# Performance work log

Measured on AMD Instinct MI355X. Metric: run time of the kernel, lower is better.

The kernel has to match this reference:

```python
import math
import jax, jax.numpy as jnp
import numpy as np

B, S, D_MODEL, H = 2, 2048, 1024, 16
HD = D_MODEL // H  # head_dim = 64


def setup_inputs() -> dict:
    key = jax.random.key(0)
    ks = jax.random.split(key, 5)
    scale = 1.0 / math.sqrt(D_MODEL)
    return {
        "x": jax.random.normal(ks[0], (B, S, D_MODEL), dtype=jnp.float32),
        "attention_mask": jnp.ones((B, S), dtype=jnp.int32),
        "causal": 1,
        "Wq": jax.random.normal(ks[1], (D_MODEL, D_MODEL), dtype=jnp.float32) * scale,
        "Wk": jax.random.normal(ks[2], (D_MODEL, D_MODEL), dtype=jnp.float32) * scale,
        "Wv": jax.random.normal(ks[3], (D_MODEL, D_MODEL), dtype=jnp.float32) * scale,
        "Wo": jax.random.normal(ks[4], (D_MODEL, D_MODEL), dtype=jnp.float32) * scale,
    }


def reference(x, attention_mask, causal, Wq, Wk, Wv, Wo):
    b, s, d = x.shape
    # QKV projections, split heads -> (b, h, s, hd)
    q = (x @ Wq).reshape(b, s, H, HD).transpose(0, 2, 1, 3)
    k = (x @ Wk).reshape(b, s, H, HD).transpose(0, 2, 1, 3)
    v = (x @ Wv).reshape(b, s, H, HD).transpose(0, 2, 1, 3)

    score = jnp.einsum("bhqd,bhkd->bhqk", q, k) / math.sqrt(HD)

    neg_inf = jnp.float32(-jnp.inf)
    if causal:
        causal_mask = jnp.tril(jnp.ones((s, s), dtype=bool))  # (s, s)
        score = jnp.where(causal_mask[None, None, :, :], score, neg_inf)
    key_mask = attention_mask.astype(bool)[:, None, None, :]  # (b,1,1,s)
    score = jnp.where(key_mask, score, neg_inf)

    attn = jax.nn.softmax(score, axis=-1)  # numerically stable (max-subtracted)
    out = jnp.einsum("bhqk,bhkd->bhqd", attn, v)  # (b,h,s,hd)
    out = out.transpose(0, 2, 1, 3).reshape(b, s, d)
    return out @ Wo
```

## Files before the change

### kernel.cpp

```cpp
#include <hip/hip_runtime.h>
#include <hip/hip_bf16.h>

#define B_  2
#define S_  2048
#define D_  1024
#define H_  16
#define HD_ 64
#define BS_ (B_*S_)

typedef __attribute__((ext_vector_type(8))) short bf16x8;
typedef __attribute__((ext_vector_type(4))) float f32x4;
typedef __attribute__((ext_vector_type(4))) float float4v;
typedef __attribute__((ext_vector_type(4))) unsigned short ushort4v;
typedef __attribute__((ext_vector_type(2))) unsigned int uint2v;

__device__ __forceinline__ unsigned short f2bf(float f) {
  union { float f; unsigned int u; } v; v.f = f;
  unsigned int u = v.u;
  return (unsigned short)((u + 0x7fffu + ((u >> 16) & 1u)) >> 16);
}
__device__ __forceinline__ float bf2f(unsigned short u) {
  union { unsigned int i; float f; } v; v.i = ((unsigned int)u) << 16; return v.f;
}
__device__ __forceinline__ unsigned int cvtpk(float lo, float hi) {
  unsigned int r;
  asm("v_cvt_pk_bf16_f32 %0, %1, %2" : "=v"(r) : "v"(lo), "v"(hi));
  return r;
}

__device__ __forceinline__ void gload16(const void* g, void* l) {
  __builtin_amdgcn_global_load_lds((const __attribute__((address_space(1))) void*)g,
                                   (__attribute__((address_space(3))) void*)l, 16, 0, 0);
}

__device__ __forceinline__ f32x4 mfma16(bf16x8 a, bf16x8 b, f32x4 c) {
  return __builtin_amdgcn_mfma_f32_16x16x32_bf16(a, b, c, 0, 0, 0);
}

__device__ __forceinline__ void store1(float* p, float v) { *p = v; }
__device__ __forceinline__ void store1(unsigned short* p, float v) { *p = f2bf(v); }

__global__ __launch_bounds__(256) void k_convert(const float* __restrict__ src,
                                                 unsigned short* __restrict__ dst, int n8) {
  int i = blockIdx.x * 256 + threadIdx.x;
  if (i >= n8) return;
  float4v a = ((const float4v*)src)[2*i];
  float4v b = ((const float4v*)src)[2*i + 1];
  union { bf16x8 v; unsigned short u[8]; } o;
#pragma unroll
  for (int j = 0; j < 4; ++j) { o.u[j] = f2bf(a[j]); o.u[4+j] = f2bf(b[j]); }
  ((bf16x8*)dst)[i] = o.v;
}

__global__ __launch_bounds__(256) void k_wt(const float* __restrict__ w0, const float* __restrict__ w1,
                                            const float* __restrict__ w2, const float* __restrict__ w3,
                                            unsigned short* __restrict__ o0, unsigned short* __restrict__ o1,
                                            unsigned short* __restrict__ o2, unsigned short* __restrict__ o3) {
  const float* w = blockIdx.z == 0 ? w0 : blockIdx.z == 1 ? w1 : blockIdx.z == 2 ? w2 : w3;
  unsigned short* o = blockIdx.z == 0 ? o0 : blockIdx.z == 1 ? o1 : blockIdx.z == 2 ? o2 : o3;
  __shared__ unsigned short til[64][68];
  const int n0 = blockIdx.x * 64, k0 = blockIdx.y * 64;
  const int t = threadIdx.x, r = t >> 4, c4 = t & 15;
#pragma unroll
  for (int i = 0; i < 4; ++i) {
    float4v v = *(const float4v*)(w + (size_t)(k0 + i*16 + r) * D_ + n0 + c4*4);
#pragma unroll
    for (int j = 0; j < 4; ++j) til[i*16 + r][c4*4 + j] = f2bf(v[j]);
  }
  __syncthreads();
#pragma unroll
  for (int i = 0; i < 4; ++i) {
    ushort4v u;
#pragma unroll
    for (int j = 0; j < 4; ++j) u[j] = til[c4*4 + j][i*16 + r];
    *(ushort4v*)(o + (size_t)(n0 + i*16 + r) * D_ + k0 + c4*4) = u;
  }
}

template <typename OutT>
__device__ __forceinline__ void gemm_body(const unsigned short* __restrict__ A,
                                          const unsigned short* __restrict__ Bt,
                                          OutT* __restrict__ C,
                                          int M, int N, int K, int mblk, int nblk) {
  __shared__ unsigned short As[128 * 64];
  __shared__ unsigned short Bs[128 * 64];
  const int tid = threadIdx.x;
  const int w = tid >> 6, lane = tid & 63;
  const int lg = lane >> 4, li = lane & 15;
  const int m0 = mblk * 128, n0 = nblk * 128;
  const int wr = (w >> 1) * 64, wc = (w & 1) * 64;
  f32x4 acc[4][4] = {};
  for (int kt = 0; kt < K; kt += 64) {
#pragma unroll
    for (int i = 0; i < 4; ++i) {
      int c = (i*4 + w) * 64 + lane;
      int r = c >> 3, kc = c & 7;
      int off = ((kc ^ (r & 7)) << 3);
      gload16(A  + (size_t)(m0 + r) * K + kt + off, (char*)As + (i*4 + w) * 1024);
      gload16(Bt + (size_t)(n0 + r) * K + kt + off, (char*)Bs + (i*4 + w) * 1024);
    }
    __syncthreads();
#pragma unroll
    for (int ks = 0; ks < 2; ++ks) {
      bf16x8 af[4], bfr[4];
#pragma unroll
      for (int m = 0; m < 4; ++m) {
        int rr = wr + m*16 + li;
        int ch = (ks*4 + lg) ^ (rr & 7);
        af[m] = *(const bf16x8*)((const char*)As + rr*128 + ch*16);
      }
#pragma unroll
      for (int n = 0; n < 4; ++n) {
        int rr = wc + n*16 + li;
        int ch = (ks*4 + lg) ^ (rr & 7);
        bfr[n] = *(const bf16x8*)((const char*)Bs + rr*128 + ch*16);
      }
#pragma unroll
      for (int m = 0; m < 4; ++m)
#pragma unroll
        for (int n = 0; n < 4; ++n)
          acc[m][n] = mfma16(af[m], bfr[n], acc[m][n]);
    }
    __syncthreads();
  }
#pragma unroll
  for (int m = 0; m < 4; ++m)
#pragma unroll
    for (int n = 0; n < 4; ++n)
#pragma unroll
      for (int j = 0; j < 4; ++j) {
        int row = m0 + wr + m*16 + lg*4 + j;
        int col = n0 + wc + n*16 + li;
        store1(&C[(size_t)row * N + col], acc[m][n][j]);
      }
}

__global__ __launch_bounds__(256, 2) void k_qkv(const unsigned short* __restrict__ xb,
    const unsigned short* __restrict__ wqt, const unsigned short* __restrict__ wkt,
    const unsigned short* __restrict__ wvt,
    unsigned short* __restrict__ Qb, unsigned short* __restrict__ Kb, unsigned short* __restrict__ Vb) {
  const unsigned short* Bt = blockIdx.z == 0 ? wqt : blockIdx.z == 1 ? wkt : wvt;
  unsigned short* C = blockIdx.z == 0 ? Qb : blockIdx.z == 1 ? Kb : Vb;
  gemm_body<unsigned short>(xb, Bt, C, BS_, D_, D_, blockIdx.x, blockIdx.y);
}

__global__ __launch_bounds__(256, 2) void k_out(const unsigned short* __restrict__ AO,
                                                const unsigned short* __restrict__ wot,
                                                float* __restrict__ out) {
  gemm_body<float>(AO, wot, out, BS_, D_, D_, blockIdx.x, blockIdx.y);
}

__global__ __launch_bounds__(256) void k_vt(const unsigned short* __restrict__ V,
                                            unsigned short* __restrict__ Vt) {
  __shared__ unsigned short til[64][68];
  const int s0 = blockIdx.x * 64, bh = blockIdx.y;
  const int b = bh >> 4, h = bh & 15;
  const int t = threadIdx.x, r = t >> 4, c4 = t & 15;
#pragma unroll
  for (int i = 0; i < 4; ++i) {
    ushort4v v = *(const ushort4v*)(V + (size_t)(b*S_ + s0 + i*16 + r) * D_ + h*HD_ + c4*4);
#pragma unroll
    for (int j = 0; j < 4; ++j) til[i*16 + r][c4*4 + j] = v[j];
  }
  __syncthreads();
#pragma unroll
  for (int i = 0; i < 4; ++i) {
    ushort4v u;
#pragma unroll
    for (int j = 0; j < 4; ++j) u[j] = til[c4*4 + j][i*16 + r];
    *(ushort4v*)(Vt + (size_t)(bh*HD_ + i*16 + r) * S_ + s0 + c4*4) = u;
  }
}

__global__ __launch_bounds__(256, 4) void k_attn(const unsigned short* __restrict__ Q,
                                                 const unsigned short* __restrict__ K,
                                                 const unsigned short* __restrict__ Vt,
                                                 unsigned short* __restrict__ AO) {
  __shared__ unsigned short Ks[2 * 64 * 64];
  __shared__ unsigned short Vs[2 * 64 * 64];
  __shared__ unsigned short Ps[4 * 16 * 64];
  const int bh = blockIdx.x;
  const int qb = 31 - blockIdx.y;
  const int b = bh >> 4, h = bh & 15;
  const int tid = threadIdx.x, w = tid >> 6, lane = tid & 63;
  const int lg = lane >> 4, li = lane & 15;
  unsigned short* Psw = Ps + w * 1024;
  const float SC2 = 0.18033688f;

  const unsigned short* qptr = Q + (size_t)(b*S_ + qb*64 + w*16 + li) * D_ + h*HD_;
  union { bf16x8 v; unsigned short u[8]; } q0u, q1u;
  q0u.v = *(const bf16x8*)(qptr + lg*8);
  q1u.v = *(const bf16x8*)(qptr + 32 + lg*8);
#pragma unroll
  for (int j = 0; j < 8; ++j) {
    q0u.u[j] = f2bf(bf2f(q0u.u[j]) * SC2);
    q1u.u[j] = f2bf(bf2f(q1u.u[j]) * SC2);
  }
  const bf16x8 qf0 = q0u.v, qf1 = q1u.v;

  int paddr[8];
#pragma unroll
  for (int kj = 0; kj < 4; ++kj)
#pragma unroll
    for (int hh = 0; hh < 2; ++hh)
      paddr[kj*2 + hh] = li*128 + (((2*kj + (lg >> 1)) ^ (li & 7)) << 4) + (lg & 1)*8 + 4*hh;
  int pboff[2];
#pragma unroll
  for (int ks = 0; ks < 2; ++ks)
    pboff[ks] = li*128 + (((ks*4 + lg) ^ (li & 7)) << 4);

  f32x4 oacc[4] = {};
  float mrow = -1e30f, lrow = 0.f;

  auto stage = [&](int bsel, int kt) {
    char* KsB = (char*)Ks + bsel * 8192;
    char* VsB = (char*)Vs + bsel * 8192;
#pragma unroll
    for (int i = 0; i < 2; ++i) {
      int c = (i*4 + w) * 64 + lane;
      int r = c >> 3, kc = c & 7;
      int off = ((kc ^ (r & 7)) << 3);
      gload16(K  + (size_t)(b*S_ + kt*64 + r) * D_ + h*HD_ + off, KsB + (i*4 + w) * 1024);
      gload16(Vt + (size_t)(bh*HD_ + r) * S_ + kt*64 + off,       VsB + (i*4 + w) * 1024);
    }
  };

  stage(0, 0);
  __syncthreads();

  for (int kt = 0; kt <= qb; ++kt) {
    const int cur = kt & 1;
    if (kt < qb) stage(cur ^ 1, kt + 1);
    const char* KsB = (const char*)Ks + cur * 8192;
    const char* VsB = (const char*)Vs + cur * 8192;

    f32x4 sc[4];
    __builtin_amdgcn_s_setprio(1);
#pragma unroll
    for (int kj = 0; kj < 4; ++kj) {
      f32x4 t = {};
      t = mfma16(*(const bf16x8*)(KsB + kj*2048 + pboff[0]), qf0, t);
      t = mfma16(*(const bf16x8*)(KsB + kj*2048 + pboff[1]), qf1, t);
      sc[kj] = t;
    }
    __builtin_amdgcn_s_setprio(0);

    if (kt == qb) {
      const int qloc = w*16 + li;
#pragma unroll
      for (int kj = 0; kj < 4; ++kj)
#pragma unroll
        for (int j = 0; j < 4; ++j)
          if (kj*16 + lg*4 + j > qloc) sc[kj][j] = -1e30f;
    }

    float mx = sc[0][0];
#pragma unroll
    for (int kj = 0; kj < 4; ++kj)
#pragma unroll
      for (int j = 0; j < 4; ++j) mx = fmaxf(mx, sc[kj][j]);
    mx = fmaxf(mx, __shfl_xor(mx, 16, 64));
    mx = fmaxf(mx, __shfl_xor(mx, 32, 64));
    const float mnew = fmaxf(mrow, mx);
    if (__any(mnew != mrow)) {
      const float alpha = exp2f(mrow - mnew);
#pragma unroll
      for (int n = 0; n < 4; ++n)
#pragma unroll
        for (int j = 0; j < 4; ++j) oacc[n][j] *= alpha;
      lrow *= alpha;
      mrow = mnew;
    }
    float rs = 0.f;
    f32x4 pv[4];
#pragma unroll
    for (int kj = 0; kj < 4; ++kj)
#pragma unroll
      for (int j = 0; j < 4; ++j) {
        float p = exp2f(sc[kj][j] - mrow);
        rs += p;
        pv[kj][j] = p;
      }
    rs += __shfl_xor(rs, 16, 64);
    rs += __shfl_xor(rs, 32, 64);
    lrow += rs;

#pragma unroll
    for (int kj = 0; kj < 4; ++kj) {
      *(unsigned int*)((char*)Psw + paddr[kj*2 + 0]) = cvtpk(pv[kj][0], pv[kj][1]);
      *(unsigned int*)((char*)Psw + paddr[kj*2 + 1]) = cvtpk(pv[kj][2], pv[kj][3]);
    }

    const bf16x8 pf0 = *(const bf16x8*)((const char*)Psw + pboff[0]);
    const bf16x8 pf1 = *(const bf16x8*)((const char*)Psw + pboff[1]);
    __builtin_amdgcn_s_setprio(1);
#pragma unroll
    for (int n = 0; n < 4; ++n) {
      oacc[n] = mfma16(*(const bf16x8*)(VsB + n*2048 + pboff[0]), pf0, oacc[n]);
      oacc[n] = mfma16(*(const bf16x8*)(VsB + n*2048 + pboff[1]), pf1, oacc[n]);
    }
    __builtin_amdgcn_s_setprio(0);
    __syncthreads();
  }

  const float inv = 1.0f / lrow;
  unsigned short* aorow = AO + (size_t)(b*S_ + qb*64 + w*16 + li) * D_ + h*HD_;
#pragma unroll
  for (int n = 0; n < 4; ++n) {
    uint2v o2;
    o2[0] = cvtpk(oacc[n][0] * inv, oacc[n][1] * inv);
    o2[1] = cvtpk(oacc[n][2] * inv, oacc[n][3] * inv);
    *(uint2v*)(aorow + n*16 + lg*4) = o2;
  }
}

extern "C" void kernel_launch(void* const* d_in, const int* in_sizes, int n_in,
                              void* d_out, int out_size, void* d_ws, size_t ws_size,
                              hipStream_t stream) {
  const float* x  = (const float*)d_in[0];
  const float* Wq = (const float*)d_in[3];
  const float* Wk = (const float*)d_in[4];
  const float* Wv = (const float*)d_in[5];
  const float* Wo = (const float*)d_in[6];
  float* out = (float*)d_out;

  unsigned short* ws  = (unsigned short*)d_ws;
  unsigned short* xb  = ws;
  unsigned short* wqt = xb  + (size_t)BS_ * D_;
  unsigned short* wkt = wqt + (size_t)D_ * D_;
  unsigned short* wvt = wkt + (size_t)D_ * D_;
  unsigned short* wot = wvt + (size_t)D_ * D_;
  unsigned short* Qb  = wot + (size_t)D_ * D_;
  unsigned short* Kb  = Qb  + (size_t)BS_ * D_;
  unsigned short* Vb  = Kb  + (size_t)BS_ * D_;
  unsigned short* Vtb = Vb  + (size_t)BS_ * D_;
  unsigned short* AO  = Vtb + (size_t)BS_ * D_;

  k_convert<<<2048, 256, 0, stream>>>(x, xb, BS_ * D_ / 8);
  k_wt<<<dim3(16, 16, 4), 256, 0, stream>>>(Wq, Wk, Wv, Wo, wqt, wkt, wvt, wot);
  k_qkv<<<dim3(32, 8, 3), 256, 0, stream>>>(xb, wqt, wkt, wvt, Qb, Kb, Vb);
  k_vt<<<dim3(32, 32), 256, 0, stream>>>(Vb, Vtb);
  k_attn<<<dim3(32, 32), 256, 0, stream>>>(Qb, Kb, Vtb, AO);
  k_out<<<dim3(32, 8), 256, 0, stream>>>(AO, wot, out);
}
```

Baseline: 115.7 us.

## Fuse prep kernels, write V transposed from GEMM, and tune attention softmax

Merges the x conversion and weight transpose kernels into one launch. The QKV GEMM now writes V directly in transposed per-head layout, which removes the separate V-transpose kernel and its extra memory round trip. The attention kernel reorders q-block scheduling to balance causal work, precomputes load offsets, uses a lazy max-rescale threshold, and defers row-sum cross-lane reduction to the end. The lazy rescale lets exponents grow by up to 2^8 before rescaling, which is a small numerical risk, and the transposed V stores are narrow strided writes.

Result: faster. 112.4 us (-2.8%).

```diff
diff --git a/kernel.cpp b/kernel.cpp
--- a/kernel.cpp
+++ b/kernel.cpp
@@ -37,29 +37,28 @@
   return __builtin_amdgcn_mfma_f32_16x16x32_bf16(a, b, c, 0, 0, 0);
 }
 
-__device__ __forceinline__ void store1(float* p, float v) { *p = v; }
-__device__ __forceinline__ void store1(unsigned short* p, float v) { *p = f2bf(v); }
-
-__global__ __launch_bounds__(256) void k_convert(const float* __restrict__ src,
-                                                 unsigned short* __restrict__ dst, int n8) {
-  int i = blockIdx.x * 256 + threadIdx.x;
-  if (i >= n8) return;
-  float4v a = ((const float4v*)src)[2*i];
-  float4v b = ((const float4v*)src)[2*i + 1];
-  union { bf16x8 v; unsigned short u[8]; } o;
-#pragma unroll
-  for (int j = 0; j < 4; ++j) { o.u[j] = f2bf(a[j]); o.u[4+j] = f2bf(b[j]); }
-  ((bf16x8*)dst)[i] = o.v;
-}
-
-__global__ __launch_bounds__(256) void k_wt(const float* __restrict__ w0, const float* __restrict__ w1,
-                                            const float* __restrict__ w2, const float* __restrict__ w3,
-                                            unsigned short* __restrict__ o0, unsigned short* __restrict__ o1,
-                                            unsigned short* __restrict__ o2, unsigned short* __restrict__ o3) {
-  const float* w = blockIdx.z == 0 ? w0 : blockIdx.z == 1 ? w1 : blockIdx.z == 2 ? w2 : w3;
-  unsigned short* o = blockIdx.z == 0 ? o0 : blockIdx.z == 1 ? o1 : blockIdx.z == 2 ? o2 : o3;
+__global__ __launch_bounds__(256) void k_prep(const float* __restrict__ x, unsigned short* __restrict__ xb,
+                                              const float* __restrict__ w0, const float* __restrict__ w1,
+                                              const float* __restrict__ w2, const float* __restrict__ w3,
+                                              unsigned short* __restrict__ o0, unsigned short* __restrict__ o1,
+                                              unsigned short* __restrict__ o2, unsigned short* __restrict__ o3) {
+  const int bid = blockIdx.x;
+  if (bid < 2048) {
+    int i = bid * 256 + threadIdx.x;
+    float4v a = ((const float4v*)x)[2*i];
+    float4v b = ((const float4v*)x)[2*i + 1];
+    union { bf16x8 v; unsigned short u[8]; } o;
+#pragma unroll
+    for (int j = 0; j < 4; ++j) { o.u[j] = f2bf(a[j]); o.u[4+j] = f2bf(b[j]); }
+    ((bf16x8*)xb)[i] = o.v;
+    return;
+  }
+  const int wid = bid - 2048;
+  const int xx = wid & 15, yy = (wid >> 4) & 15, zz = wid >> 8;
+  const float* w = zz == 0 ? w0 : zz == 1 ? w1 : zz == 2 ? w2 : w3;
+  unsigned short* o = zz == 0 ? o0 : zz == 1 ? o1 : zz == 2 ? o2 : o3;
   __shared__ unsigned short til[64][68];
-  const int n0 = blockIdx.x * 64, k0 = blockIdx.y * 64;
+  const int n0 = xx * 64, k0 = yy * 64;
   const int t = threadIdx.x, r = t >> 4, c4 = t & 15;
 #pragma unroll
   for (int i = 0; i < 4; ++i) {
@@ -77,7 +76,7 @@
   }
 }
 
-template <typename OutT>
+template <int MODE, typename OutT>
 __device__ __forceinline__ void gemm_body(const unsigned short* __restrict__ A,
                                           const unsigned short* __restrict__ Bt,
                                           OutT* __restrict__ C,
@@ -126,50 +125,44 @@
 #pragma unroll
   for (int m = 0; m < 4; ++m)
 #pragma unroll
-    for (int n = 0; n < 4; ++n)
-#pragma unroll
-      for (int j = 0; j < 4; ++j) {
-        int row = m0 + wr + m*16 + lg*4 + j;
-        int col = n0 + wc + n*16 + li;
-        store1(&C[(size_t)row * N + col], acc[m][n][j]);
+    for (int n = 0; n < 4; ++n) {
+      if (MODE == 2) {
+        int gr = m0 + wr + m*16 + lg*4;
+        int gc = n0 + wc + n*16 + li;
+        int bb = gr >> 11, ss = gr & 2047, hh = gc >> 6, dd = gc & 63;
+        unsigned short* p = (unsigned short*)C + ((size_t)((bb*H_ + hh)*HD_ + dd)) * S_ + ss;
+        uint2v o2;
+        o2[0] = cvtpk(acc[m][n][0], acc[m][n][1]);
+        o2[1] = cvtpk(acc[m][n][2], acc[m][n][3]);
+        *(uint2v*)p = o2;
+      } else {
+#pragma unroll
+        for (int j = 0; j < 4; ++j) {
+          int row = m0 + wr + m*16 + lg*4 + j;
+          int col = n0 + wc + n*16 + li;
+          if (MODE == 1) ((float*)C)[(size_t)row * N + col] = acc[m][n][j];
+          else ((unsigned short*)C)[(size_t)row * N + col] = f2bf(acc[m][n][j]);
+        }
       }
+    }
 }
 
 __global__ __launch_bounds__(256, 2) void k_qkv(const unsigned short* __restrict__ xb,
     const unsigned short* __restrict__ wqt, const unsigned short* __restrict__ wkt,
     const unsigned short* __restrict__ wvt,
-    unsigned short* __restrict__ Qb, unsigned short* __restrict__ Kb, unsigned short* __restrict__ Vb) {
-  const unsigned short* Bt = blockIdx.z == 0 ? wqt : blockIdx.z == 1 ? wkt : wvt;
-  unsigned short* C = blockIdx.z == 0 ? Qb : blockIdx.z == 1 ? Kb : Vb;
-  gemm_body<unsigned short>(xb, Bt, C, BS_, D_, D_, blockIdx.x, blockIdx.y);
+    unsigned short* __restrict__ Qb, unsigned short* __restrict__ Kb, unsigned short* __restrict__ Vtb) {
+  const int z = blockIdx.z;
+  if (z == 2) {
+    gemm_body<2, unsigned short>(xb, wvt, Vtb, BS_, D_, D_, blockIdx.x, blockIdx.y);
+  } else {
+    gemm_body<0, unsigned short>(xb, z ? wkt : wqt, z ? Kb : Qb, BS_, D_, D_, blockIdx.x, blockIdx.y);
+  }
 }
 
 __global__ __launch_bounds__(256, 2) void k_out(const unsigned short* __restrict__ AO,
                                                 const unsigned short* __restrict__ wot,
                                                 float* __restrict__ out) {
-  gemm_body<float>(AO, wot, out, BS_, D_, D_, blockIdx.x, blockIdx.y);
-}
-
-__global__ __launch_bounds__(256) void k_vt(const unsigned short* __restrict__ V,
-                                            unsigned short* __restrict__ Vt) {
-  __shared__ unsigned short til[64][68];
-  const int s0 = blockIdx.x * 64, bh = blockIdx.y;
-  const int b = bh >> 4, h = bh & 15;
-  const int t = threadIdx.x, r = t >> 4, c4 = t & 15;
-#pragma unroll
-  for (int i = 0; i < 4; ++i) {
-    ushort4v v = *(const ushort4v*)(V + (size_t)(b*S_ + s0 + i*16 + r) * D_ + h*HD_ + c4*4);
-#pragma unroll
-    for (int j = 0; j < 4; ++j) til[i*16 + r][c4*4 + j] = v[j];
-  }
-  __syncthreads();
-#pragma unroll
-  for (int i = 0; i < 4; ++i) {
-    ushort4v u;
-#pragma unroll
-    for (int j = 0; j < 4; ++j) u[j] = til[c4*4 + j][i*16 + r];
-    *(ushort4v*)(Vt + (size_t)(bh*HD_ + i*16 + r) * S_ + s0 + c4*4) = u;
-  }
+  gemm_body<1, float>(AO, wot, out, BS_, D_, D_, blockIdx.x, blockIdx.y);
 }
 
 __global__ __launch_bounds__(256, 4) void k_attn(const unsigned short* __restrict__ Q,
@@ -180,7 +173,8 @@
   __shared__ unsigned short Vs[2 * 64 * 64];
   __shared__ unsigned short Ps[4 * 16 * 64];
   const int bh = blockIdx.x;
-  const int qb = 31 - blockIdx.y;
+  const int y = blockIdx.y;
+  const int qb = (y < 8) ? 31 - y : (y < 16) ? y - 8 : (y < 24) ? 39 - y : y - 16;
   const int b = bh >> 4, h = bh & 15;
   const int tid = threadIdx.x, w = tid >> 6, lane = tid & 63;
   const int lg = lane >> 4, li = lane & 15;
@@ -209,28 +203,41 @@
   for (int ks = 0; ks < 2; ++ks)
     pboff[ks] = li*128 + (((ks*4 + lg) ^ (li & 7)) << 4);
 
+  int kofs[2], vofs[2], lofs[2];
+#pragma unroll
+  for (int i = 0; i < 2; ++i) {
+    int c = (i*4 + w) * 64 + lane;
+    int r = c >> 3, kc = c & 7;
+    int off = ((kc ^ (r & 7)) << 3);
+    kofs[i] = r * D_ + off;
+    vofs[i] = r * S_ + off;
+    lofs[i] = (i*4 + w) * 1024;
+  }
+  const unsigned short* kg = K  + (size_t)(b*S_) * D_ + h*HD_;
+  const unsigned short* vg = Vt + (size_t)bh * HD_ * S_;
+
   f32x4 oacc[4] = {};
   float mrow = -1e30f, lrow = 0.f;
 
-  auto stage = [&](int bsel, int kt) {
+  auto stage = [&](int bsel, const unsigned short* kp, const unsigned short* vp) {
     char* KsB = (char*)Ks + bsel * 8192;
     char* VsB = (char*)Vs + bsel * 8192;
 #pragma unroll
     for (int i = 0; i < 2; ++i) {
-      int c = (i*4 + w) * 64 + lane;
-      int r = c >> 3, kc = c & 7;
-      int off = ((kc ^ (r & 7)) << 3);
-      gload16(K  + (size_t)(b*S_ + kt*64 + r) * D_ + h*HD_ + off, KsB + (i*4 + w) * 1024);
-      gload16(Vt + (size_t)(bh*HD_ + r) * S_ + kt*64 + off,       VsB + (i*4 + w) * 1024);
+      gload16(kp + kofs[i], KsB + lofs[i]);
+      gload16(vp + vofs[i], VsB + lofs[i]);
     }
   };
 
-  stage(0, 0);
+  stage(0, kg, vg);
   __syncthreads();
 
   for (int kt = 0; kt <= qb; ++kt) {
     const int cur = kt & 1;
-    if (kt < qb) stage(cur ^ 1, kt + 1);
+    if (kt < qb) {
+      kg += 64 * D_; vg += 64;
+      stage(cur ^ 1, kg, vg);
+    }
     const char* KsB = (const char*)Ks + cur * 8192;
     const char* VsB = (const char*)Vs + cur * 8192;
 
@@ -254,15 +261,16 @@
           if (kj*16 + lg*4 + j > qloc) sc[kj][j] = -1e30f;
     }
 
-    float mx = sc[0][0];
-#pragma unroll
-    for (int kj = 0; kj < 4; ++kj)
-#pragma unroll
-      for (int j = 0; j < 4; ++j) mx = fmaxf(mx, sc[kj][j]);
-    mx = fmaxf(mx, __shfl_xor(mx, 16, 64));
+    float a0 = fmaxf(fmaxf(sc[0][0], sc[0][1]), sc[0][2]);
+    float a1 = fmaxf(fmaxf(sc[0][3], sc[1][0]), sc[1][1]);
+    float a2 = fmaxf(fmaxf(sc[1][2], sc[1][3]), sc[2][0]);
+    float a3 = fmaxf(fmaxf(sc[2][1], sc[2][2]), sc[2][3]);
+    float a4 = fmaxf(fmaxf(sc[3][0], sc[3][1]), sc[3][2]);
+    float mx = fmaxf(fmaxf(fmaxf(a0, a1), fmaxf(a2, a3)), fmaxf(a4, sc[3][3]));
+    mx = fmaxf(mx, __int_as_float(__builtin_amdgcn_ds_swizzle(__float_as_int(mx), 0x401F)));
     mx = fmaxf(mx, __shfl_xor(mx, 32, 64));
-    const float mnew = fmaxf(mrow, mx);
-    if (__any(mnew != mrow)) {
+    if (__any(mx > mrow + 8.f)) {
+      const float mnew = fmaxf(mrow, mx);
       const float alpha = exp2f(mrow - mnew);
 #pragma unroll
       for (int n = 0; n < 4; ++n)
@@ -281,8 +289,6 @@
         rs += p;
         pv[kj][j] = p;
       }
-    rs += __shfl_xor(rs, 16, 64);
-    rs += __shfl_xor(rs, 32, 64);
     lrow += rs;
 
 #pragma unroll
@@ -303,6 +309,8 @@
     __syncthreads();
   }
 
+  lrow += __int_as_float(__builtin_amdgcn_ds_swizzle(__float_as_int(lrow), 0x401F));
+  lrow += __shfl_xor(lrow, 32, 64);
   const float inv = 1.0f / lrow;
   unsigned short* aorow = AO + (size_t)(b*S_ + qb*64 + w*16 + li) * D_ + h*HD_;
 #pragma unroll
@@ -332,14 +340,11 @@
   unsigned short* wot = wvt + (size_t)D_ * D_;
   unsigned short* Qb  = wot + (size_t)D_ * D_;
   unsigned short* Kb  = Qb  + (size_t)BS_ * D_;
-  unsigned short* Vb  = Kb  + (size_t)BS_ * D_;
-  unsigned short* Vtb = Vb  + (size_t)BS_ * D_;
+  unsigned short* Vtb = Kb  + (size_t)BS_ * D_;
   unsigned short* AO  = Vtb + (size_t)BS_ * D_;
 
-  k_convert<<<2048, 256, 0, stream>>>(x, xb, BS_ * D_ / 8);
-  k_wt<<<dim3(16, 16, 4), 256, 0, stream>>>(Wq, Wk, Wv, Wo, wqt, wkt, wvt, wot);
-  k_qkv<<<dim3(32, 8, 3), 256, 0, stream>>>(xb, wqt, wkt, wvt, Qb, Kb, Vb);
-  k_vt<<<dim3(32, 32), 256, 0, stream>>>(Vb, Vtb);
+  k_prep<<<3072, 256, 0, stream>>>(x, xb, Wq, Wk, Wv, Wo, wqt, wkt, wvt, wot);
+  k_qkv<<<dim3(32, 8, 3), 256, 0, stream>>>(xb, wqt, wkt, wvt, Qb, Kb, Vtb);
   k_attn<<<dim3(32, 32), 256, 0, stream>>>(Qb, Kb, Vtb, AO);
   k_out<<<dim3(32, 8), 256, 0, stream>>>(AO, wot, out);
 }
```
